# Kernel tuning notes

Measured on AMD Instinct MI355X. Metric: run time of the kernel, lower is better.

The kernel has to match this reference:

```python
import jax, jax.numpy as jnp
import numpy as np


def _ste(q, x):
    # straight-through estimator: forward = q, gradient = identity w.r.t. x
    return x + jax.lax.stop_gradient(q - x)


def quant_w(w, bit_w=8):
    # symmetric per-tensor weight quantization fused into QConv2d
    qmax = 2.0 ** (bit_w - 1) - 1.0
    scale = jnp.max(jnp.abs(w)) / qmax
    q = jnp.clip(jnp.round(w / scale), -qmax, qmax) * scale
    return _ste(q, w)


def quant_a(x, bit_a=8):
    # unsigned activation quantizer: clamp to [0,1], uniform bit_a levels
    n = 2.0 ** bit_a - 1.0
    xc = jnp.clip(x, 0.0, 1.0)
    q = jnp.round(xc * n) / n
    return _ste(q, xc)


def exp_norm2d(x, gamma, beta, eps=1e-5):
    # instance-style norm: per (N, C) statistics over spatial dims, affine
    mean = jnp.mean(x, axis=(2, 3), keepdims=True)
    var = jnp.var(x, axis=(2, 3), keepdims=True)
    xn = (x - mean) * jax.lax.rsqrt(var + eps)
    return xn * gamma[None, :, None, None] + beta[None, :, None, None]


def qconv(x, w, stride, pad, bit_w=8):
    wq = quant_w(w, bit_w)
    return jax.lax.conv_general_dilated(
        x, wq, window_strides=(stride, stride),
        padding=[(pad, pad), (pad, pad)],
        dimension_numbers=('NCHW', 'OIHW', 'NCHW'))


def setup_inputs() -> dict:
    key = jax.random.key(0)
    ks = jax.random.split(key, 4)
    C_in, C_out, H = 256, 512, 56
    return {
        'x': jax.random.normal(ks[0], (32, C_in, H, H), jnp.float32),
        'w1': jax.random.normal(ks[1], (C_out, C_in, 3, 3), jnp.float32) * 0.05,
        'g1': jnp.ones((C_out,), jnp.float32),
        'b1': jnp.zeros((C_out,), jnp.float32),
        'w2': jax.random.normal(ks[2], (C_out, C_out, 3, 3), jnp.float32) * 0.05,
        'g2': jnp.ones((C_out,), jnp.float32),
        'b2': jnp.zeros((C_out,), jnp.float32),
        'wp': jax.random.normal(ks[3], (C_out, C_in, 1, 1), jnp.float32) * 0.05,
        'gp': jnp.ones((C_out,), jnp.float32),
        'bp': jnp.zeros((C_out,), jnp.float32),
    }


def reference(x, w1, g1, b1, w2, g2, b2, wp, gp, bp):
    # main branch: QConv(s2) -> ExpNorm -> act quant -> QConv(s1) -> ExpNorm
    h = qconv(x, w1, stride=2, pad=1)
    h = exp_norm2d(h, g1, b1)
    h = quant_a(h, bit_a=8)
    h = qconv(h, w2, stride=1, pad=1)
    h = exp_norm2d(h, g2, b2)
    # projection shortcut: QConv 1x1 stride 2 -> ExpNorm
    s = qconv(x, wp, stride=2, pad=0)
    s = exp_norm2d(s, gp, bp)
    return h + s
```

## Files before the change

### kernel.cpp

```cpp
#include <hip/hip_runtime.h>
#include <cstdint>
#include <cstddef>


typedef unsigned short ushort_t;
typedef __attribute__((ext_vector_type(8))) short bf16x8;
typedef __attribute__((ext_vector_type(4))) float f32x4;
typedef __attribute__((ext_vector_type(4))) int i32x4;

#define NB   32
#define C_IN 256
#define HIN  56
#define CO   512
#define OHW  784
#define OWD  28
#define MTOT (NB * OHW)

constexpr size_t OFF_XH   = 0;
constexpr size_t OFF_A1   = OFF_XH  + 51380224;
constexpr size_t OFF_H2   = OFF_A1  + 25690112;
constexpr size_t OFF_S    = OFF_H2  + 51380224;
constexpr size_t OFF_WT1  = OFF_S   + 51380224;
constexpr size_t OFF_WT2  = OFF_WT1 + 2359296;
constexpr size_t OFF_WTP  = OFF_WT2 + 4718592;
constexpr size_t OFF_PSUM = OFF_WTP + 262144;
constexpr size_t OFF_A1N  = OFF_PSUM + 2097152;
constexpr size_t OFF_B1N  = OFF_A1N + 65536;
constexpr size_t OFF_A2N  = OFF_B1N + 65536;
constexpr size_t OFF_B2N  = OFF_A2N + 65536;
constexpr size_t OFF_APN  = OFF_B2N + 65536;
constexpr size_t OFF_BPN  = OFF_APN + 65536;
constexpr size_t OFF_MX   = OFF_BPN + 65536;
constexpr size_t OFF_ZB   = OFF_MX  + 16;
constexpr size_t OFF_CS   = OFF_ZB  + 2048;

__device__ __forceinline__ ushort_t f2bf(float f) {
    unsigned u = __float_as_uint(f);
    u += 0x7FFFu + ((u >> 16) & 1u);
    return (ushort_t)(u >> 16);
}
__device__ __forceinline__ float bf2f(ushort_t u) {
    return __uint_as_float(((unsigned)u) << 16);
}

__device__ __forceinline__ void async_copy16(const void* g, const void* l) {
    auto gp = (const __attribute__((address_space(1))) unsigned int*)(uintptr_t)g;
    auto lp = (__attribute__((address_space(3))) unsigned int*)(unsigned int)(uintptr_t)l;
    __builtin_amdgcn_global_load_lds(gp, lp, 16, 0, 0);
}

__global__ void to_nhwc_k(const float* __restrict__ x, ushort_t* __restrict__ xh) {
    __shared__ float tile[64][33];
    const int wt0 = blockIdx.x * 32;
    const int ct0 = blockIdx.y * 64;
    const int nh  = blockIdx.z;
    const int n = nh / HIN, h = nh - n * HIN;
    {
        const int tx = threadIdx.x & 31;
        const int ty = threadIdx.x >> 5;
        const int w  = wt0 + tx;
#pragma unroll
        for (int j = 0; j < 8; ++j) {
            int cl = ty + j * 8;
            if (w < HIN)
                tile[cl][tx] = x[(((size_t)n * C_IN + ct0 + cl) * HIN + h) * HIN + w];
        }
    }
    __syncthreads();
    {
        const int tc = threadIdx.x & 63;
        const int tw = threadIdx.x >> 6;
#pragma unroll
        for (int j = 0; j < 8; ++j) {
            int wl = tw + j * 4;
            int w  = wt0 + wl;
            if (w < HIN)
                xh[(((size_t)n * HIN + h) * HIN + w) * C_IN + ct0 + tc] =
                    f2bf(tile[tc][wl]);
        }
    }
}

__global__ void absmax3_k(const float* __restrict__ w1, int n1,
                          const float* __restrict__ w2, int n2,
                          const float* __restrict__ wp, int np,
                          unsigned* out) {
    const float* w; int nelem;
    if (blockIdx.y == 0)      { w = w1; nelem = n1; }
    else if (blockIdx.y == 1) { w = w2; nelem = n2; }
    else                      { w = wp; nelem = np; }
    int stride = gridDim.x * blockDim.x;
    float m = 0.f;
    for (int i = blockIdx.x * blockDim.x + threadIdx.x; i < nelem; i += stride)
        m = fmaxf(m, fabsf(w[i]));
#pragma unroll
    for (int off = 32; off > 0; off >>= 1)
        m = fmaxf(m, __shfl_down(m, off));
    if ((threadIdx.x & 63) == 0) atomicMax(out + blockIdx.y, __float_as_uint(m));
}

template <int CO_, int CI_, int KHW_>
__global__ void quantw_k(const float* __restrict__ w, const unsigned* __restrict__ mx,
                         ushort_t* __restrict__ wt) {
    const int total = KHW_ * CO_ * CI_;
    int idx = blockIdx.x * 256 + threadIdx.x;
    if (idx >= total) return;
    float scale = __uint_as_float(*mx) * (1.0f / 127.0f);
    float inv   = scale > 0.f ? 1.0f / scale : 0.f;
    int khw = idx / (CO_ * CI_);
    int r   = idx - khw * (CO_ * CI_);
    int co  = r / CI_;
    int ci  = r - co * CI_;
    float v  = w[((size_t)co * CI_ + ci) * KHW_ + khw];
    float qv = rintf(v * inv);
    qv = fminf(127.f, fmaxf(-127.f, qv));
    wt[idx] = f2bf(qv * scale);
}

__global__ void quantw_i8_k(const float* __restrict__ w, const unsigned* __restrict__ mx,
                            signed char* __restrict__ wt) {
    const int total = 9 * CO * CO;
    int idx = blockIdx.x * 256 + threadIdx.x;
    if (idx >= total) return;
    float scale = __uint_as_float(*mx) * (1.0f / 127.0f);
    float inv   = scale > 0.f ? 1.0f / scale : 0.f;
    int khw = idx / (CO * CO);
    int r   = idx - khw * (CO * CO);
    int co  = r / CO;
    int ci  = r - co * CO;
    float v  = w[((size_t)co * CO + ci) * 9 + khw];
    float qv = rintf(v * inv);
    qv = fminf(127.f, fmaxf(-127.f, qv));
    wt[idx] = (signed char)(int)qv;
}

__global__ void colsum_k(const signed char* __restrict__ wt, float* __restrict__ cs) {
    const int khw = blockIdx.x;
    const int co  = blockIdx.y * 32 + (threadIdx.x & 31);
    const int cig = threadIdx.x >> 5;
    const signed char* p = wt + ((size_t)khw * CO + co) * CO + cig * 64;
    int s = 0;
#pragma unroll
    for (int i = 0; i < 64; ++i) s += p[i];
    __shared__ int red[8][32];
    red[cig][threadIdx.x & 31] = s;
    __syncthreads();
    if (cig == 0) {
        int tot = 0;
#pragma unroll
        for (int g = 0; g < 8; ++g) tot += red[g][threadIdx.x & 31];
        cs[khw * CO + co] = (float)tot;
    }
}

template <int CIN, int KH, int KW, int STRIDE, int PAD, int IH, int IW>
__launch_bounds__(512, 2)
__global__ void conv8p_k(const ushort_t* __restrict__ xin,
                         const ushort_t* __restrict__ wt,
                         ushort_t* __restrict__ out,
                         const ushort_t* __restrict__ zbuf,
                         float* __restrict__ psum, float* __restrict__ pss) {
    constexpr int BK  = 64;
    constexpr int CKT = CIN / BK;
    constexpr int KT  = KH * KW * CKT;

    __shared__ alignas(16) short As[2 * 256 * BK];
    __shared__ alignas(16) short Bs[2 * 256 * BK];

    const int tid  = threadIdx.x;
    const int lane = tid & 63;
    const int wv   = tid >> 6;
    const int wm   = wv >> 2;
    const int wn   = wv & 3;
    const int lrow = lane & 15;
    const int lq   = lane >> 4;
    const int sw   = lrow & 7;

    const int bid = blockIdx.x;
    const int xcd = bid & 7;
    const int j   = bid >> 3;
    const int wg  = (xcd < 4 ? xcd * 25 : 100 + (xcd - 4) * 24) + j;
    const int m0  = (wg >> 1) * 256;
    const int co0 = (wg & 1) * 256;

    const int arow = tid >> 3;
    const int ach  = tid & 7;
    long abase[4]; unsigned amask[4]; int bco[4];
#pragma unroll
    for (int c = 0; c < 4; ++c) {
        int row = c * 64 + arow;
        int m   = m0 + row;
        int n   = m / OHW;
        int sp  = m - n * OHW;
        int oh  = sp / OWD, ow = sp - oh * OWD;
        int ihb = oh * STRIDE - PAD, iwb = ow * STRIDE - PAD;
        int swz = (ach ^ (row & 7)) * 8;
        abase[c] = ((long)n * (IH * IW) + (long)ihb * IW + iwb) * CIN + swz;
        unsigned mk = 0;
#pragma unroll
        for (int kh = 0; kh < KH; ++kh)
#pragma unroll
            for (int kw = 0; kw < KW; ++kw) {
                int ih = ihb + kh, iw = iwb + kw;
                if ((unsigned)ih < (unsigned)IH && (unsigned)iw < (unsigned)IW)
                    mk |= 1u << (kh * KW + kw);
            }
        amask[c] = mk;
        bco[c]   = (co0 + row) * CIN + swz;
    }

    auto stageA = [&](int c, int nb, long aoff, int khw) {
        const ushort_t* src = ((amask[c] >> khw) & 1)
            ? xin + (abase[c] + aoff) : zbuf;
        async_copy16(src, (const void*)&As[nb * 16384 + c * 4096 + wv * 512]);
    };
    auto stageB = [&](int c, int nb, int boff) {
        async_copy16(wt + (boff + bco[c]),
                     (const void*)&Bs[nb * 16384 + c * 4096 + wv * 512]);
    };

    f32x4 acc[8][4];
#pragma unroll
    for (int a = 0; a < 8; ++a)
#pragma unroll
        for (int b = 0; b < 4; ++b) acc[a][b] = {0.f, 0.f, 0.f, 0.f};

    stageB(0, 0, 0); stageB(1, 0, 0); stageB(2, 0, 0); stageB(3, 0, 0);
    stageA(0, 0, 0, 0); stageA(1, 0, 0, 0); stageA(2, 0, 0, 0); stageA(3, 0, 0, 0);
    asm volatile("s_waitcnt vmcnt(0)" ::: "memory");
    __builtin_amdgcn_s_barrier();

    int  khw_n = 0, kw_n = 0, ck_n = 1;
    long aoff_n = BK;
    int  boff_n = BK;

    int cur = 0;
    for (int t = 0; t < KT; ++t) {
        const bool hn = (t + 1 < KT);
        const int  nb = cur ^ 1;
        const short* Acur = &As[cur * 16384];
        const short* Bcur = &Bs[cur * 16384];

        if (hn) {
            stageB(0, nb, boff_n); stageB(1, nb, boff_n);
            stageB(2, nb, boff_n); stageB(3, nb, boff_n);
            stageA(0, nb, aoff_n, khw_n); stageA(1, nb, aoff_n, khw_n);
            stageA(2, nb, aoff_n, khw_n); stageA(3, nb, aoff_n, khw_n);
        }
        __builtin_amdgcn_sched_barrier(0);

        bf16x8 af[4][2], bfr[2][2][2];

#pragma unroll
        for (int mi = 0; mi < 4; ++mi) {
            const int row = wm * 128 + mi * 16 + lrow;
#pragma unroll
            for (int ks = 0; ks < 2; ++ks) {
                const int ch = ((ks * 4 + lq) ^ sw) * 8;
                af[mi][ks] = *(const bf16x8*)&Acur[row * BK + ch];
            }
        }
#pragma unroll
        for (int qn = 0; qn < 2; ++qn)
#pragma unroll
            for (int ni = 0; ni < 2; ++ni) {
                const int row = wn * 64 + qn * 32 + ni * 16 + lrow;
#pragma unroll
                for (int ks = 0; ks < 2; ++ks) {
                    const int ch = ((ks * 4 + lq) ^ sw) * 8;
                    bfr[qn][ni][ks] = *(const bf16x8*)&Bcur[row * BK + ch];
                }
            }
#pragma unroll
        for (int mi = 0; mi < 4; ++mi)
#pragma unroll
            for (int qn = 0; qn < 2; ++qn)
#pragma unroll
                for (int ni = 0; ni < 2; ++ni)
#pragma unroll
                    for (int ks = 0; ks < 2; ++ks)
                        acc[mi][qn * 2 + ni] =
                            __builtin_amdgcn_mfma_f32_16x16x32_bf16(
                                af[mi][ks], bfr[qn][ni][ks],
                                acc[mi][qn * 2 + ni], 0, 0, 0);

#pragma unroll
        for (int mi = 0; mi < 4; ++mi) {
            const int row = wm * 128 + 64 + mi * 16 + lrow;
#pragma unroll
            for (int ks = 0; ks < 2; ++ks) {
                const int ch = ((ks * 4 + lq) ^ sw) * 8;
                af[mi][ks] = *(const bf16x8*)&Acur[row * BK + ch];
            }
        }
#pragma unroll
        for (int mi = 0; mi < 4; ++mi)
#pragma unroll
            for (int qn = 0; qn < 2; ++qn)
#pragma unroll
                for (int ni = 0; ni < 2; ++ni)
#pragma unroll
                    for (int ks = 0; ks < 2; ++ks)
                        acc[4 + mi][qn * 2 + ni] =
                            __builtin_amdgcn_mfma_f32_16x16x32_bf16(
                                af[mi][ks], bfr[qn][ni][ks],
                                acc[4 + mi][qn * 2 + ni], 0, 0, 0);

        asm volatile("s_waitcnt vmcnt(0)" ::: "memory");
        __builtin_amdgcn_sched_barrier(0);
        __builtin_amdgcn_s_barrier();

        if (hn) {
            ck_n++;
            if (ck_n == CKT) {
                ck_n = 0; khw_n++; kw_n++;
                if (kw_n == KW) { kw_n = 0; aoff_n += (long)(IW - KW) * CIN + BK; }
                else            { aoff_n += BK; }
                boff_n += (CO - 1) * CIN + BK;
            } else {
                aoff_n += BK; boff_n += BK;
            }
        }
        cur ^= 1;
    }

    const int mb = m0 + wm * 128 + lq * 4;
    const int cb = co0 + wn * 64 + lrow;
#pragma unroll
    for (int mi = 0; mi < 8; ++mi)
#pragma unroll
        for (int ni = 0; ni < 4; ++ni)
#pragma unroll
            for (int r = 0; r < 4; ++r)
                out[(size_t)(mb + mi * 16 + r) * CO + (cb + ni * 16)] =
                    f2bf(acc[mi][ni][r]);

    const int n0 = m0 / OHW;
    const int mS = (n0 + 1) * OHW;
    float sv[2][4], qv[2][4];
#pragma unroll
    for (int g = 0; g < 2; ++g)
#pragma unroll
        for (int ni = 0; ni < 4; ++ni) { sv[g][ni] = 0.f; qv[g][ni] = 0.f; }
#pragma unroll
    for (int mi = 0; mi < 8; ++mi)
#pragma unroll
        for (int ni = 0; ni < 4; ++ni)
#pragma unroll
            for (int r = 0; r < 4; ++r) {
                float v = acc[mi][ni][r];
                int m = mb + mi * 16 + r;
                int g = (m >= mS) ? 1 : 0;
                sv[g][ni] += v; qv[g][ni] += v * v;
            }
#pragma unroll
    for (int d = 16; d <= 32; d <<= 1)
#pragma unroll
        for (int g = 0; g < 2; ++g)
#pragma unroll
            for (int ni = 0; ni < 4; ++ni) {
                sv[g][ni] += __shfl_xor(sv[g][ni], d);
                qv[g][ni] += __shfl_xor(qv[g][ni], d);
            }
    if (lq == 0) {
        const bool split = (mS < m0 + 256);
#pragma unroll
        for (int ni = 0; ni < 4; ++ni) {
            atomicAdd(&psum[n0 * CO + cb + ni * 16], sv[0][ni]);
            atomicAdd(&pss [n0 * CO + cb + ni * 16], qv[0][ni]);
            if (split) {
                atomicAdd(&psum[(n0 + 1) * CO + cb + ni * 16], sv[1][ni]);
                atomicAdd(&pss [(n0 + 1) * CO + cb + ni * 16], qv[1][ni]);
            }
        }
    }
}

__launch_bounds__(512, 4)
__global__ void conv_i8_k(const signed char* __restrict__ xin,
                          const signed char* __restrict__ wt,
                          const float* __restrict__ colsum,
                          const unsigned* __restrict__ mxp,
                          ushort_t* __restrict__ out,
                          const signed char* __restrict__ zbuf,
                          float* __restrict__ psum, float* __restrict__ pss) {
    constexpr int CIN = 512, BK = 64, CKT = 8, KT = 72;
    constexpr int IH = 28, IW = 28;

    __shared__ alignas(16) signed char As[2 * 128 * BK];
    __shared__ alignas(16) signed char Bs[2 * 128 * BK];

    const int tid  = threadIdx.x;
    const int lane = tid & 63;
    const int wv   = tid >> 6;
    const int wm   = wv >> 2;
    const int wn   = wv & 3;
    const int lrow = lane & 15;
    const int lq   = lane >> 4;

    const int bid = blockIdx.x;
    const int wg  = (bid & 7) * 98 + (bid >> 3);
    const int m0  = (wg >> 2) * 128;
    const int co0 = (wg & 3) * 128;

    const int arow = tid >> 2;
    const int ach  = tid & 3;
    const int fsw  = (arow >> 1) & 3;
    int abase; unsigned amask; int bco;
    {
        int m   = m0 + arow;
        int n   = m / OHW;
        int sp  = m - n * OHW;
        int oh  = sp / OWD, ow = sp - oh * OWD;
        int ihb = oh - 1, iwb = ow - 1;
        int swz = (ach ^ fsw) * 16;
        abase = (n * (IH * IW) + ihb * IW + iwb) * CIN + swz;
        unsigned mk = 0;
#pragma unroll
        for (int kh = 0; kh < 3; ++kh)
#pragma unroll
            for (int kw = 0; kw < 3; ++kw) {
                int ih = ihb + kh, iw = iwb + kw;
                if ((unsigned)ih < (unsigned)IH && (unsigned)iw < (unsigned)IW)
                    mk |= 1u << (kh * 3 + kw);
            }
        amask = mk;
        bco = (co0 + arow) * CIN + swz;
    }

    auto stageA = [&](int nb, int aoff, int khw) {
        const signed char* src = ((amask >> khw) & 1)
            ? xin + (abase + aoff) : zbuf;
        async_copy16(src, (const void*)&As[nb * 8192 + wv * 1024]);
    };
    auto stageB = [&](int nb, int boff) {
        async_copy16(wt + (boff + bco),
                     (const void*)&Bs[nb * 8192 + wv * 1024]);
    };

    i32x4 acc[4][2];
#pragma unroll
    for (int a = 0; a < 4; ++a)
#pragma unroll
        for (int b = 0; b < 2; ++b) acc[a][b] = {0, 0, 0, 0};

    stageB(0, 0);
    stageA(0, 0, 0);
    asm volatile("s_waitcnt vmcnt(0)" ::: "memory");
    __builtin_amdgcn_s_barrier();

    int khw_n = 0, kw_n = 0, ck_n = 1;
    int aoff_n = BK;
    int boff_n = BK;

    int cur = 0;
    for (int t = 0; t < KT; ++t) {
        const bool hn = (t + 1 < KT);
        const int  nb = cur ^ 1;
        const signed char* Acur = &As[cur * 8192];
        const signed char* Bcur = &Bs[cur * 8192];

        if (hn) { stageB(nb, boff_n); stageA(nb, aoff_n, khw_n); }
        __builtin_amdgcn_sched_barrier(0);

        i32x4 af[4], bfr[2];
#pragma unroll
        for (int mi = 0; mi < 4; ++mi) {
            const int row = wm * 64 + mi * 16 + lrow;
            af[mi] = *(const i32x4*)&Acur[row * BK + ((lq ^ ((row >> 1) & 3)) * 16)];
        }
#pragma unroll
        for (int ni = 0; ni < 2; ++ni) {
            const int row = wn * 32 + ni * 16 + lrow;
            bfr[ni] = *(const i32x4*)&Bcur[row * BK + ((lq ^ ((row >> 1) & 3)) * 16)];
        }
#pragma unroll
        for (int mi = 0; mi < 4; ++mi)
#pragma unroll
            for (int ni = 0; ni < 2; ++ni)
                acc[mi][ni] = __builtin_amdgcn_mfma_i32_16x16x64_i8(
                    af[mi], bfr[ni], acc[mi][ni], 0, 0, 0);

        asm volatile("s_waitcnt vmcnt(0)" ::: "memory");
        __builtin_amdgcn_sched_barrier(0);
        __builtin_amdgcn_s_barrier();

        if (hn) {
            ck_n++;
            if (ck_n == CKT) {
                ck_n = 0; khw_n++; kw_n++;
                if (kw_n == 3) { kw_n = 0; aoff_n += (IW - 3) * CIN + BK; }
                else           { aoff_n += BK; }
                boff_n += (CO - 1) * CIN + BK;
            } else {
                aoff_n += BK; boff_n += BK;
            }
        }
        cur ^= 1;
    }

    const int mb = m0 + wm * 64 + lq * 4;
    const int cb = co0 + wn * 32 + lrow;
    const float scale = __uint_as_float(*mxp) * (1.0f / 127.0f);
    const float sc    = scale * (1.0f / 255.0f);
    const float c128  = 128.0f * sc;

    float Sall[2], Sr0[2], Sr2[2], Sc0[2], Sc2[2], K0[2], K2[2], K6[2], K8[2];
#pragma unroll
    for (int ni = 0; ni < 2; ++ni) {
        float cs[9];
#pragma unroll
        for (int k = 0; k < 9; ++k) cs[k] = colsum[k * CO + cb + ni * 16];
        Sall[ni] = cs[0]+cs[1]+cs[2]+cs[3]+cs[4]+cs[5]+cs[6]+cs[7]+cs[8];
        Sr0[ni] = cs[0]+cs[1]+cs[2];  Sr2[ni] = cs[6]+cs[7]+cs[8];
        Sc0[ni] = cs[0]+cs[3]+cs[6];  Sc2[ni] = cs[2]+cs[5]+cs[8];
        K0[ni] = cs[0]; K2[ni] = cs[2]; K6[ni] = cs[6]; K8[ni] = cs[8];
    }

    const int n0 = m0 / OHW;
    const int mS = (n0 + 1) * OHW;
    float sv[2][2], qvv[2][2];
#pragma unroll
    for (int g = 0; g < 2; ++g)
#pragma unroll
        for (int ni = 0; ni < 2; ++ni) { sv[g][ni] = 0.f; qvv[g][ni] = 0.f; }

#pragma unroll
    for (int mi = 0; mi < 4; ++mi)
#pragma unroll
        for (int r = 0; r < 4; ++r) {
            const int m  = mb + mi * 16 + r;
            const int n  = m / OHW;
            const int sp = m - n * OHW;
            const int oh = sp / OWD, ow = sp - oh * OWD;
            const int g  = (m >= mS) ? 1 : 0;
#pragma unroll
            for (int ni = 0; ni < 2; ++ni) {
                float T = Sall[ni];
                if (oh == 0)       T -= Sr0[ni];
                if (oh == OWD - 1) T -= Sr2[ni];
                if (ow == 0)       T -= Sc0[ni];
                if (ow == OWD - 1) T -= Sc2[ni];
                if (oh == 0 && ow == 0)             T += K0[ni];
                if (oh == 0 && ow == OWD - 1)       T += K2[ni];
                if (oh == OWD - 1 && ow == 0)       T += K6[ni];
                if (oh == OWD - 1 && ow == OWD - 1) T += K8[ni];
                float val = sc * (float)acc[mi][ni][r] + c128 * T;
                out[(size_t)m * CO + (cb + ni * 16)] = f2bf(val);
                sv[g][ni] += val; qvv[g][ni] += val * val;
            }
        }
#pragma unroll
    for (int d = 16; d <= 32; d <<= 1)
#pragma unroll
        for (int g = 0; g < 2; ++g)
#pragma unroll
            for (int ni = 0; ni < 2; ++ni) {
                sv[g][ni]  += __shfl_xor(sv[g][ni], d);
                qvv[g][ni] += __shfl_xor(qvv[g][ni], d);
            }
    if (lq == 0) {
        const bool split = (mS < m0 + 128);
#pragma unroll
        for (int ni = 0; ni < 2; ++ni) {
            atomicAdd(&psum[n0 * CO + cb + ni * 16], sv[0][ni]);
            atomicAdd(&pss [n0 * CO + cb + ni * 16], qvv[0][ni]);
            if (split) {
                atomicAdd(&psum[(n0 + 1) * CO + cb + ni * 16], sv[1][ni]);
                atomicAdd(&pss [(n0 + 1) * CO + cb + ni * 16], qvv[1][ni]);
            }
        }
    }
}

__global__ void statsf3_k(const float* __restrict__ ps0, const float* __restrict__ qs0,
                          const float* __restrict__ g0, const float* __restrict__ bb0,
                          float* __restrict__ ao0, float* __restrict__ bo0,
                          const float* __restrict__ ps1, const float* __restrict__ qs1,
                          const float* __restrict__ g1, const float* __restrict__ bb1,
                          float* __restrict__ ao1, float* __restrict__ bo1,
                          const float* __restrict__ ps2, const float* __restrict__ qs2,
                          const float* __restrict__ g2, const float* __restrict__ bb2,
                          float* __restrict__ ao2, float* __restrict__ bo2) {
    const float *ps, *qs, *g, *bb; float *ao, *bo;
    if (blockIdx.y == 0)      { ps = ps0; qs = qs0; g = g0; bb = bb0; ao = ao0; bo = bo0; }
    else if (blockIdx.y == 1) { ps = ps1; qs = qs1; g = g1; bb = bb1; ao = ao1; bo = bo1; }
    else                      { ps = ps2; qs = qs2; g = g2; bb = bb2; ao = ao2; bo = bo2; }
    int idx = blockIdx.x * 256 + threadIdx.x;
    int c = idx & 511;
    float s  = ps[idx];
    float ss = qs[idx];
    float mean = s * (1.0f / 784.0f);
    float var  = ss * (1.0f / 784.0f) - mean * mean;
    float rstd = rsqrtf(var + 1e-5f);
    float a = rstd * g[c];
    ao[idx] = a;
    bo[idx] = bb[c] - mean * a;
}

__global__ void norm_quant_i8_k(const ushort_t* __restrict__ h, const float* __restrict__ a_,
                                const float* __restrict__ b_, signed char* __restrict__ o) {
    int idx = blockIdx.x * 256 + threadIdx.x;
    int row = idx >> 6;
    int c0  = (idx & 63) * 8;
    int n   = row / OHW;
    bf16x8 v = ((const bf16x8*)h)[idx];
    const float* ap = a_ + n * CO + c0;
    const float* bp = b_ + n * CO + c0;
    unsigned lo = 0, hi = 0;
#pragma unroll
    for (int k = 0; k < 8; ++k) {
        float f = bf2f((ushort_t)v[k]) * ap[k] + bp[k];
        float kq = rintf(fminf(fmaxf(f, 0.f), 1.f) * 255.f);
        int s8 = (int)kq - 128;
        unsigned b = (unsigned)(s8 & 0xFF);
        if (k < 4) lo |= b << (8 * k);
        else       hi |= b << (8 * (k - 4));
    }
    ((uint2*)o)[idx] = make_uint2(lo, hi);
}

__global__ void final_k(const ushort_t* __restrict__ h2, const ushort_t* __restrict__ s,
                        const float* __restrict__ a2, const float* __restrict__ b2,
                        const float* __restrict__ ap_, const float* __restrict__ bp_,
                        float* __restrict__ out) {
    __shared__ float tile[64][33];
    const int sp0 = blockIdx.x * 32;
    const int c0  = blockIdx.y * 64;
    const int n   = blockIdx.z;
    const int tx  = threadIdx.x & 31;
    const int ty  = threadIdx.x >> 5;
#pragma unroll
    for (int j = 0; j < 4; ++j) {
        int spl = ty + j * 8;
        int sp  = sp0 + spl;
        if (sp < OHW) {
            int c = c0 + tx * 2;
            size_t ix = ((size_t)n * OHW + sp) * CO + c;
            int ci = n * CO + c;
            ushort2 vh = *(const ushort2*)&h2[ix];
            ushort2 vs = *(const ushort2*)&s[ix];
            tile[tx * 2][spl] =
                bf2f(vh.x) * a2[ci] + b2[ci] + bf2f(vs.x) * ap_[ci] + bp_[ci];
            tile[tx * 2 + 1][spl] =
                bf2f(vh.y) * a2[ci + 1] + b2[ci + 1] + bf2f(vs.y) * ap_[ci + 1] + bp_[ci + 1];
        }
    }
    __syncthreads();
    const int sp = sp0 + tx;
#pragma unroll
    for (int j = 0; j < 8; ++j) {
        int cl = ty + j * 8;
        if (sp < OHW)
            out[((size_t)n * CO + c0 + cl) * OHW + sp] = tile[cl][tx];
    }
}

extern "C" void kernel_launch(void* const* d_in, const int* in_sizes, int n_in,
                              void* d_out, int out_size, void* d_ws, size_t ws_size,
                              hipStream_t stream) {
    const float* x  = (const float*)d_in[0];
    const float* w1 = (const float*)d_in[1];
    const float* g1 = (const float*)d_in[2];
    const float* b1 = (const float*)d_in[3];
    const float* w2 = (const float*)d_in[4];
    const float* g2 = (const float*)d_in[5];
    const float* b2 = (const float*)d_in[6];
    const float* wp = (const float*)d_in[7];
    const float* gp = (const float*)d_in[8];
    const float* bp = (const float*)d_in[9];
    float* out = (float*)d_out;
    char* ws = (char*)d_ws;

    ushort_t*    xh    = (ushort_t*)(ws + OFF_XH);
    signed char* a1    = (signed char*)(ws + OFF_A1);
    ushort_t*    h2    = (ushort_t*)(ws + OFF_H2);
    ushort_t*    sbuf  = (ushort_t*)(ws + OFF_S);
    ushort_t*    wt1   = (ushort_t*)(ws + OFF_WT1);
    signed char* wt2i  = (signed char*)(ws + OFF_WT2);
    ushort_t*    wtp   = (ushort_t*)(ws + OFF_WTP);
    float*    psum1 = (float*)(ws + OFF_PSUM);
    float*    pss1  = (float*)(ws + OFF_PSUM + 65536);
    float*    psum2 = (float*)(ws + OFF_PSUM + 131072);
    float*    pss2  = (float*)(ws + OFF_PSUM + 196608);
    float*    psump = (float*)(ws + OFF_PSUM + 262144);
    float*    pssp  = (float*)(ws + OFF_PSUM + 327680);
    float*    a1n  = (float*)(ws + OFF_A1N);
    float*    b1n  = (float*)(ws + OFF_B1N);
    float*    a2n  = (float*)(ws + OFF_A2N);
    float*    b2n  = (float*)(ws + OFF_B2N);
    float*    apn  = (float*)(ws + OFF_APN);
    float*    bpn  = (float*)(ws + OFF_BPN);
    unsigned* mx   = (unsigned*)(ws + OFF_MX);
    ushort_t* zb   = (ushort_t*)(ws + OFF_ZB);
    float*    cs   = (float*)(ws + OFF_CS);
    ushort_t* h1   = (ushort_t*)out;

    hipMemsetAsync(ws + OFF_MX, 0, 16 + 2048, stream);
    hipMemsetAsync(ws + OFF_PSUM, 0, 393216, stream);

    to_nhwc_k<<<dim3(2, 4, NB * HIN), 256, 0, stream>>>(x, xh);
    absmax3_k<<<dim3(512, 3), 256, 0, stream>>>(w1, CO * C_IN * 9,
                                                w2, CO * CO * 9,
                                                wp, C_IN * CO, mx);
    quantw_k<CO, C_IN, 9><<<dim3(4608), 256, 0, stream>>>(w1, mx + 0, wt1);
    quantw_i8_k<<<dim3(9216), 256, 0, stream>>>(w2, mx + 1, wt2i);
    quantw_k<CO, C_IN, 1><<<dim3(512), 256, 0, stream>>>(wp, mx + 2, wtp);
    colsum_k<<<dim3(9, 16), 256, 0, stream>>>(wt2i, cs);

    conv8p_k<C_IN, 3, 3, 2, 1, HIN, HIN>
        <<<dim3(196), 512, 0, stream>>>(xh, wt1, h1, (const ushort_t*)zb, psum1, pss1);
    statsf3_k<<<dim3(64, 1), 256, 0, stream>>>(psum1, pss1, g1, b1, a1n, b1n,
                                               psum1, pss1, g1, b1, a1n, b1n,
                                               psum1, pss1, g1, b1, a1n, b1n);
    norm_quant_i8_k<<<dim3(MTOT * CO / 8 / 256), 256, 0, stream>>>(h1, a1n, b1n, a1);

    conv_i8_k<<<dim3(784), 512, 0, stream>>>(a1, wt2i, cs, mx + 1, h2,
                                             (const signed char*)zb, psum2, pss2);
    conv8p_k<C_IN, 1, 1, 2, 0, HIN, HIN>
        <<<dim3(196), 512, 0, stream>>>(xh, wtp, sbuf, (const ushort_t*)zb, psump, pssp);

    statsf3_k<<<dim3(64, 2), 256, 0, stream>>>(psum2, pss2, g2, b2, a2n, b2n,
                                               psump, pssp, gp, bp, apn, bpn,
                                               psum2, pss2, g2, b2, a2n, b2n);

    final_k<<<dim3(25, 8, NB), 256, 0, stream>>>(h2, sbuf, a2n, b2n, apn, bpn, out);
}
```

Before: 342.5 us.

## Enlarge int8 conv tile to 256x256 and fuse weight colsum into quantization

The int8 3x3 conv now runs 1024-thread blocks computing 256x256 output tiles (196 blocks instead of 784), with each wave holding a 4x4 grid of MFMA accumulators and doubled LDS staging buffers. The block-to-XCD mapping is adjusted for the uneven 196-block count. Separately, the per-column weight sum is computed inside the int8 weight quantization kernel with a wave shuffle reduction plus float atomics, which removes the colsum kernel launch. The bigger tile cuts global reloads of A and B per output, but it raises register and LDS pressure, leaves fewer blocks than the GPU has CUs, and relies on a zeroed colsum buffer through the enlarged memset.

Measured after the change: 320.5 us. -6.4%, faster.

```diff
diff --git a/kernel.cpp b/kernel.cpp
--- a/kernel.cpp
+++ b/kernel.cpp
@@ -118,10 +118,8 @@
 }
 
 __global__ void quantw_i8_k(const float* __restrict__ w, const unsigned* __restrict__ mx,
-                            signed char* __restrict__ wt) {
-    const int total = 9 * CO * CO;
+                            signed char* __restrict__ wt, float* __restrict__ cs) {
     int idx = blockIdx.x * 256 + threadIdx.x;
-    if (idx >= total) return;
     float scale = __uint_as_float(*mx) * (1.0f / 127.0f);
     float inv   = scale > 0.f ? 1.0f / scale : 0.f;
     int khw = idx / (CO * CO);
@@ -131,26 +129,13 @@
     float v  = w[((size_t)co * CO + ci) * 9 + khw];
     float qv = rintf(v * inv);
     qv = fminf(127.f, fmaxf(-127.f, qv));
-    wt[idx] = (signed char)(int)qv;
-}
-
-__global__ void colsum_k(const signed char* __restrict__ wt, float* __restrict__ cs) {
-    const int khw = blockIdx.x;
-    const int co  = blockIdx.y * 32 + (threadIdx.x & 31);
-    const int cig = threadIdx.x >> 5;
-    const signed char* p = wt + ((size_t)khw * CO + co) * CO + cig * 64;
-    int s = 0;
-#pragma unroll
-    for (int i = 0; i < 64; ++i) s += p[i];
-    __shared__ int red[8][32];
-    red[cig][threadIdx.x & 31] = s;
-    __syncthreads();
-    if (cig == 0) {
-        int tot = 0;
-#pragma unroll
-        for (int g = 0; g < 8; ++g) tot += red[g][threadIdx.x & 31];
-        cs[khw * CO + co] = (float)tot;
-    }
+    int iq = (int)qv;
+    wt[idx] = (signed char)iq;
+    int s = iq;
+#pragma unroll
+    for (int off = 32; off > 0; off >>= 1)
+        s += __shfl_down(s, off);
+    if ((threadIdx.x & 63) == 0) atomicAdd(&cs[khw * CO + co], (float)s);
 }
 
 template <int CIN, int KH, int KW, int STRIDE, int PAD, int IH, int IW>
@@ -376,7 +361,7 @@
     }
 }
 
-__launch_bounds__(512, 4)
+__launch_bounds__(1024, 4)
 __global__ void conv_i8_k(const signed char* __restrict__ xin,
                           const signed char* __restrict__ wt,
                           const float* __restrict__ colsum,
@@ -387,8 +372,8 @@
     constexpr int CIN = 512, BK = 64, CKT = 8, KT = 72;
     constexpr int IH = 28, IW = 28;
 
-    __shared__ alignas(16) signed char As[2 * 128 * BK];
-    __shared__ alignas(16) signed char Bs[2 * 128 * BK];
+    __shared__ alignas(16) signed char As[2 * 256 * BK];
+    __shared__ alignas(16) signed char Bs[2 * 256 * BK];
 
     const int tid  = threadIdx.x;
     const int lane = tid & 63;
@@ -399,13 +384,14 @@
     const int lq   = lane >> 4;
 
     const int bid = blockIdx.x;
-    const int wg  = (bid & 7) * 98 + (bid >> 3);
-    const int m0  = (wg >> 2) * 128;
-    const int co0 = (wg & 3) * 128;
+    const int xcd = bid & 7;
+    const int j   = bid >> 3;
+    const int wg  = (xcd < 4 ? xcd * 25 : 100 + (xcd - 4) * 24) + j;
+    const int m0  = (wg >> 1) * 256;
+    const int co0 = (wg & 1) * 256;
 
     const int arow = tid >> 2;
     const int ach  = tid & 3;
-    const int fsw  = (arow >> 1) & 3;
     int abase; unsigned amask; int bco;
     {
         int m   = m0 + arow;
@@ -413,7 +399,7 @@
         int sp  = m - n * OHW;
         int oh  = sp / OWD, ow = sp - oh * OWD;
         int ihb = oh - 1, iwb = ow - 1;
-        int swz = (ach ^ fsw) * 16;
+        int swz = (ach ^ ((arow >> 1) & 3)) * 16;
         abase = (n * (IH * IW) + ihb * IW + iwb) * CIN + swz;
         unsigned mk = 0;
 #pragma unroll
@@ -431,18 +417,17 @@
     auto stageA = [&](int nb, int aoff, int khw) {
         const signed char* src = ((amask >> khw) & 1)
             ? xin + (abase + aoff) : zbuf;
-        async_copy16(src, (const void*)&As[nb * 8192 + wv * 1024]);
+        async_copy16(src, (const void*)&As[nb * 16384 + wv * 1024]);
     };
     auto stageB = [&](int nb, int boff) {
-        async_copy16(wt + (boff + bco),
-                     (const void*)&Bs[nb * 8192 + wv * 1024]);
+        async_copy16(wt + (boff + bco), (const void*)&Bs[nb * 16384 + wv * 1024]);
     };
 
-    i32x4 acc[4][2];
+    i32x4 acc[4][4];
 #pragma unroll
     for (int a = 0; a < 4; ++a)
 #pragma unroll
-        for (int b = 0; b < 2; ++b) acc[a][b] = {0, 0, 0, 0};
+        for (int b = 0; b < 4; ++b) acc[a][b] = {0, 0, 0, 0};
 
     stageB(0, 0);
     stageA(0, 0, 0);
@@ -457,27 +442,27 @@
     for (int t = 0; t < KT; ++t) {
         const bool hn = (t + 1 < KT);
         const int  nb = cur ^ 1;
-        const signed char* Acur = &As[cur * 8192];
-        const signed char* Bcur = &Bs[cur * 8192];
+        const signed char* Acur = &As[cur * 16384];
+        const signed char* Bcur = &Bs[cur * 16384];
 
         if (hn) { stageB(nb, boff_n); stageA(nb, aoff_n, khw_n); }
         __builtin_amdgcn_sched_barrier(0);
 
-        i32x4 af[4], bfr[2];
+        i32x4 af[4], bfr[4];
 #pragma unroll
         for (int mi = 0; mi < 4; ++mi) {
             const int row = wm * 64 + mi * 16 + lrow;
             af[mi] = *(const i32x4*)&Acur[row * BK + ((lq ^ ((row >> 1) & 3)) * 16)];
         }
 #pragma unroll
-        for (int ni = 0; ni < 2; ++ni) {
-            const int row = wn * 32 + ni * 16 + lrow;
+        for (int ni = 0; ni < 4; ++ni) {
+            const int row = wn * 64 + ni * 16 + lrow;
             bfr[ni] = *(const i32x4*)&Bcur[row * BK + ((lq ^ ((row >> 1) & 3)) * 16)];
         }
 #pragma unroll
         for (int mi = 0; mi < 4; ++mi)
 #pragma unroll
-            for (int ni = 0; ni < 2; ++ni)
+            for (int ni = 0; ni < 4; ++ni)
                 acc[mi][ni] = __builtin_amdgcn_mfma_i32_16x16x64_i8(
                     af[mi], bfr[ni], acc[mi][ni], 0, 0, 0);
 
@@ -500,14 +485,14 @@
     }
 
     const int mb = m0 + wm * 64 + lq * 4;
-    const int cb = co0 + wn * 32 + lrow;
+    const int cb = co0 + wn * 64 + lrow;
     const float scale = __uint_as_float(*mxp) * (1.0f / 127.0f);
     const float sc    = scale * (1.0f / 255.0f);
     const float c128  = 128.0f * sc;
 
-    float Sall[2], Sr0[2], Sr2[2], Sc0[2], Sc2[2], K0[2], K2[2], K6[2], K8[2];
-#pragma unroll
-    for (int ni = 0; ni < 2; ++ni) {
+    float Sall[4], Sr0[4], Sr2[4], Sc0[4], Sc2[4], K0[4], K2[4], K6[4], K8[4];
+#pragma unroll
+    for (int ni = 0; ni < 4; ++ni) {
         float cs[9];
 #pragma unroll
         for (int k = 0; k < 9; ++k) cs[k] = colsum[k * CO + cb + ni * 16];
@@ -519,11 +504,11 @@
 
     const int n0 = m0 / OHW;
     const int mS = (n0 + 1) * OHW;
-    float sv[2][2], qvv[2][2];
+    float sv[2][4], qvv[2][4];
 #pragma unroll
     for (int g = 0; g < 2; ++g)
 #pragma unroll
-        for (int ni = 0; ni < 2; ++ni) { sv[g][ni] = 0.f; qvv[g][ni] = 0.f; }
+        for (int ni = 0; ni < 4; ++ni) { sv[g][ni] = 0.f; qvv[g][ni] = 0.f; }
 
 #pragma unroll
     for (int mi = 0; mi < 4; ++mi)
@@ -535,7 +520,7 @@
             const int oh = sp / OWD, ow = sp - oh * OWD;
             const int g  = (m >= mS) ? 1 : 0;
 #pragma unroll
-            for (int ni = 0; ni < 2; ++ni) {
+            for (int ni = 0; ni < 4; ++ni) {
                 float T = Sall[ni];
                 if (oh == 0)       T -= Sr0[ni];
                 if (oh == OWD - 1) T -= Sr2[ni];
@@ -555,14 +540,14 @@
 #pragma unroll
         for (int g = 0; g < 2; ++g)
 #pragma unroll
-            for (int ni = 0; ni < 2; ++ni) {
+            for (int ni = 0; ni < 4; ++ni) {
                 sv[g][ni]  += __shfl_xor(sv[g][ni], d);
                 qvv[g][ni] += __shfl_xor(qvv[g][ni], d);
             }
     if (lq == 0) {
-        const bool split = (mS < m0 + 128);
-#pragma unroll
-        for (int ni = 0; ni < 2; ++ni) {
+        const bool split = (mS < m0 + 256);
+#pragma unroll
+        for (int ni = 0; ni < 4; ++ni) {
             atomicAdd(&psum[n0 * CO + cb + ni * 16], sv[0][ni]);
             atomicAdd(&pss [n0 * CO + cb + ni * 16], qvv[0][ni]);
             if (split) {
@@ -696,7 +681,7 @@
     float*    cs   = (float*)(ws + OFF_CS);
     ushort_t* h1   = (ushort_t*)out;
 
-    hipMemsetAsync(ws + OFF_MX, 0, 16 + 2048, stream);
+    hipMemsetAsync(ws + OFF_MX, 0, 16 + 2048 + 18432, stream);
     hipMemsetAsync(ws + OFF_PSUM, 0, 393216, stream);
 
     to_nhwc_k<<<dim3(2, 4, NB * HIN), 256, 0, stream>>>(x, xh);
@@ -704,9 +689,8 @@
                                                 w2, CO * CO * 9,
                                                 wp, C_IN * CO, mx);
     quantw_k<CO, C_IN, 9><<<dim3(4608), 256, 0, stream>>>(w1, mx + 0, wt1);
-    quantw_i8_k<<<dim3(9216), 256, 0, stream>>>(w2, mx + 1, wt2i);
+    quantw_i8_k<<<dim3(9216), 256, 0, stream>>>(w2, mx + 1, wt2i, cs);
     quantw_k<CO, C_IN, 1><<<dim3(512), 256, 0, stream>>>(wp, mx + 2, wtp);
-    colsum_k<<<dim3(9, 16), 256, 0, stream>>>(wt2i, cs);
 
     conv8p_k<C_IN, 3, 3, 2, 1, HIN, HIN>
         <<<dim3(196), 512, 0, stream>>>(xh, wt1, h1, (const ushort_t*)zb, psum1, pss1);
@@ -715,8 +699,8 @@
                                                psum1, pss1, g1, b1, a1n, b1n);
     norm_quant_i8_k<<<dim3(MTOT * CO / 8 / 256), 256, 0, stream>>>(h1, a1n, b1n, a1);
 
-    conv_i8_k<<<dim3(784), 512, 0, stream>>>(a1, wt2i, cs, mx + 1, h2,
-                                             (const signed char*)zb, psum2, pss2);
+    conv_i8_k<<<dim3(196), 1024, 0, stream>>>(a1, wt2i, cs, mx + 1, h2,
+                                              (const signed char*)zb, psum2, pss2);
     conv8p_k<C_IN, 1, 1, 2, 0, HIN, HIN>
         <<<dim3(196), 512, 0, stream>>>(xh, wtp, sbuf, (const ushort_t*)zb, psump, pssp);
 
```
